# Kernel optimization log

Hardware: AMD Instinct MI355X
Metric: run time of the kernel (lower is better)

## Reference

```python
import jax, jax.numpy as jnp
import numpy as np

B, S, HID = 2, 2048, 1024
H = 16
D = HID // H  # 64
SCALE = 1.0 / float(np.sqrt(D))


def setup_inputs() -> dict:
    key = jax.random.key(0)
    ks = jax.random.split(key, 12)
    s = 0.02
    return {
        "query": jax.random.normal(ks[0], (B, S, HID), jnp.float32),
        "key": jax.random.normal(ks[1], (B, S, HID), jnp.float32),
        "value": jax.random.normal(ks[2], (B, S, HID), jnp.float32),
        "attention_mask": jnp.ones((B, S, S), jnp.int32),
        "Wq": jax.random.normal(ks[3], (HID, HID), jnp.float32) * s,
        "bq": jnp.zeros((HID,), jnp.float32),
        "Wk": jax.random.normal(ks[4], (HID, HID), jnp.float32) * s,
        "bk": jnp.zeros((HID,), jnp.float32),
        "Wv": jax.random.normal(ks[5], (HID, HID), jnp.float32) * s,
        "bv": jnp.zeros((HID,), jnp.float32),
        "Wo": jax.random.normal(ks[6], (HID, HID), jnp.float32) * s,
        "bo": jnp.zeros((HID,), jnp.float32),
    }


def _split_heads(x):  # [B,S,HID] -> [B,H,S,D]
    b, s, _ = x.shape
    return x.reshape(b, s, H, D).transpose(0, 2, 1, 3)


def reference(query, key, value, attention_mask, Wq, bq, Wk, bk, Wv, bv, Wo, bo):
    # Projections (torch Linear: x @ W.T + b)
    Q = _split_heads(query @ Wq.T + bq)
    K = _split_heads(key @ Wk.T + bk)
    V = _split_heads(value @ Wv.T + bv)
    # Full attention; chunking in the original is math-equivalent (softmax over full key axis per chunk)
    scores = jnp.einsum("bhqd,bhkd->bhqk", Q, K) * SCALE
    scores = jnp.where(attention_mask[:, None, :, :] == 0, jnp.float32(-1e9), scores)
    attn = jax.nn.softmax(scores, axis=-1)  # dropout is identity in eval mode
    ctx = jnp.einsum("bhqk,bhkd->bhqd", attn, V)
    ctx = ctx.transpose(0, 2, 1, 3).reshape(query.shape[0], query.shape[1], HID)
    out = ctx @ Wo.T + bo
    # module returns a dummy uniform attention-weight tensor
    attn_weights = jnp.full((query.shape[0], H, S, S), 1.0 / S, dtype=query.dtype)
    return (out, attn_weights)
```

## Files before the change

kernel.cpp:

```cpp
#include <hip/hip_runtime.h>

typedef float f4v __attribute__((ext_vector_type(4)));
typedef float f8v __attribute__((ext_vector_type(8)));
typedef short s4v __attribute__((ext_vector_type(4)));
typedef short s8v __attribute__((ext_vector_type(8)));
typedef __bf16 bf4t __attribute__((ext_vector_type(4)));
typedef __bf16 bf8t __attribute__((ext_vector_type(8)));
typedef unsigned short u16;
typedef unsigned int u32;

#define S_LEN 2048
#define HIDN 1024
#define NH 16
#define HD 64
#define QS 0.180336879f
#define DTH 11.5415603f
#define FILLV 0.00048828125f

__device__ __forceinline__ u16 f2bf(float f) {
  return __builtin_bit_cast(u16, (__bf16)f);
}

__device__ __forceinline__ s8v cvt8(f4v x, f4v y) {
  const f8v f = {x[0], x[1], x[2], x[3], y[0], y[1], y[2], y[3]};
  return __builtin_bit_cast(s8v, __builtin_convertvector(f, bf8t));
}

__device__ __forceinline__ s4v cvt4(f4v x) {
  return __builtin_bit_cast(s4v, __builtin_convertvector(x, bf4t));
}

__device__ __forceinline__ f4v mfma16(s8v a, s8v b, f4v c) {
  return __builtin_amdgcn_mfma_f32_16x16x32_bf16(
      __builtin_bit_cast(bf8t, a), __builtin_bit_cast(bf8t, b), c, 0, 0, 0);
}

__device__ __forceinline__ void gl16(const void* g, void* l) {
  __builtin_amdgcn_global_load_lds((const __attribute__((address_space(1))) u32*)g,
                                   (__attribute__((address_space(3))) u32*)l, 16, 0, 0);
}

#define FILL_DECL(nblk)                                        \
  const f4v fvv = (f4v){FILLV, FILLV, FILLV, FILLV};           \
  f4v* fp = fillb + (size_t)bid * 256 + threadIdx.x;           \
  f4v* const fpe = fillb + fill4;                               \
  const size_t FT = (size_t)(nblk) * 256;

#define FILL_STORE()                                           \
  do { if (fp < fpe) __builtin_nontemporal_store(fvv, fp);     \
       fp += FT; } while (0)

struct PrepArgs { const float* w[4]; u16* d[4]; const int* mask; unsigned* pm; unsigned* flg; };

__global__ __launch_bounds__(256) void prep(PrepArgs a) {
  const int y = blockIdx.y;
  const int tid = threadIdx.x;
  if (y < 4) {
    const float* s = a.w[y];
    u16* d = a.d[y];
#pragma unroll
    for (int j = 0; j < 2; ++j) {
      const int i = blockIdx.x * 256 + tid + j * 65536;
      const f4v x0 = ((const f4v*)s)[2 * i];
      const f4v x1 = ((const f4v*)s)[2 * i + 1];
      ((s8v*)d)[i] = cvt8(x0, x1);
    }
  } else {
    const int lane = tid & 63;
    const size_t base = (size_t)(y - 4) * 2097152;
    bool anyz = false;
    for (int j = 0; j < 32; ++j) {
      const size_t i = base + (size_t)blockIdx.x * 256 + tid + (size_t)j * 65536;
      const unsigned long long bb = __ballot(a.mask[i] != 0);
      if (lane == 0) a.pm[i >> 5] = (unsigned)bb;
      if (lane == 32) a.pm[i >> 5] = (unsigned)(bb >> 32);
      anyz |= (bb != ~0ull);
    }
    if (anyz && lane == 0) a.flg[0] = 1u;
  }
}

struct QkvArgs {
  const float* A[3]; const u16* W[3]; const float* bias[3]; u16* out[3];
  f4v* fillb; size_t fill4;
};

__global__ __launch_bounds__(256, 3) void gemm_qkv(QkvArgs ga) {
  __shared__ __align__(16) u16 As[128 * 32];
  __shared__ __align__(16) u16 Bs[128 * 32];
  const int p = blockIdx.x;
  const int xcd = p & 7;
  const int ii = p >> 3;
  const int ytile = xcd * 12 + (ii >> 3);
  const int xt = ii & 7;
  const int id = ytile >> 5;
  const int tid = threadIdx.x;
  const int lane = tid & 63;
  const int wv = tid >> 6;
  const int wm = wv >> 1, wn = wv & 1;
  const int g = lane >> 4, l15 = lane & 15;
  const int m0 = (ytile & 31) * 128, n0 = xt * 128;
  const int bid = p;
  f4v* fillb = ga.fillb;
  const size_t fill4 = ga.fill4;
  FILL_DECL(768);

  f4v acc[4][4];
#pragma unroll
  for (int i = 0; i < 4; ++i)
#pragma unroll
    for (int j = 0; j < 4; ++j) acc[i][j] = (f4v){0.f, 0.f, 0.f, 0.f};

  const int ar = tid >> 1;
  const int ac = (tid & 1) * 16;
  const float* ap = ga.A[id] + (size_t)(m0 + ar) * HIDN + ac;
  const u16* bp0 = ga.W[id] + (size_t)(n0 + (tid >> 2)) * HIDN + (tid & 3) * 8;
  const u16* bp1 = bp0 + (size_t)64 * HIDN;
  u16* bsl0 = Bs + tid * 8;
  u16* bsl1 = Bs + 2048 + tid * 8;
  u16* asl = As + ar * 32 + ac;

  for (int kt = 0; kt < HIDN; kt += 32) {
    const f4v a0 = ((const f4v*)(ap + kt))[0];
    const f4v a1 = ((const f4v*)(ap + kt))[1];
    const f4v a2 = ((const f4v*)(ap + kt))[2];
    const f4v a3 = ((const f4v*)(ap + kt))[3];
    __syncthreads();
    gl16(bp0 + kt, bsl0);
    gl16(bp1 + kt, bsl1);
    *(s8v*)asl = cvt8(a0, a1);
    *(s8v*)(asl + 8) = cvt8(a2, a3);
    __syncthreads();
    FILL_STORE();
    FILL_STORE();
    s8v af[4], bfv[4];
#pragma unroll
    for (int i = 0; i < 4; ++i)
      af[i] = *(const s8v*)(As + (wm * 64 + i * 16 + l15) * 32 + g * 8);
#pragma unroll
    for (int j = 0; j < 4; ++j)
      bfv[j] = *(const s8v*)(Bs + (wn * 64 + j * 16 + l15) * 32 + g * 8);
#pragma unroll
    for (int i = 0; i < 4; ++i)
#pragma unroll
      for (int j = 0; j < 4; ++j) acc[i][j] = mfma16(af[i], bfv[j], acc[i][j]);
  }

  const float* bias = ga.bias[id];
  u16* out = ga.out[id];
  const int mode2 = (id == 2);
  const float osc = (id == 0) ? QS : 1.0f;
#pragma unroll
  for (int i = 0; i < 4; ++i) {
#pragma unroll
    for (int j = 0; j < 4; ++j) {
      const int mb = m0 + wm * 64 + i * 16 + g * 4;
      const int n = n0 + wn * 64 + j * 16 + l15;
      const float bv = bias[n];
#pragma unroll
      for (int r = 0; r < 4; ++r) {
        const int m = mb + r;
        const float v = (acc[i][j][r] + bv) * osc;
        const int b = m >> 11, s = m & 2047, h = n >> 6, d = n & 63;
        if (mode2) {
          out[((size_t)(b * NH + h) * HD + d) * S_LEN + s] = f2bf(v);
        } else {
          out[(((size_t)(b * NH + h) * S_LEN + s) << 6) + d] = f2bf(v);
        }
      }
    }
  }
}

__global__ __launch_bounds__(256, 4) void attn_fused(
    const u16* __restrict__ Qb, const u16* __restrict__ Kb,
    const u16* __restrict__ Vtb, u16* __restrict__ ctxb,
    const unsigned* __restrict__ pm, const unsigned* __restrict__ flg,
    f4v* __restrict__ fillb, const size_t fill4) {
  __shared__ __align__(16) u16 Ks[64 * 64];
  __shared__ __align__(16) u16 Vs[64 * 64];
  __shared__ __align__(16) u16 Ps[4][16 * 64];
  __shared__ unsigned mw[64][2];

  const int p = blockIdx.x;
  const int xcd = p & 7;
  const int ii = p >> 3;
  const int bh = xcd * 4 + (ii >> 5);
  const int q0 = (ii & 31) * 64;
  const int tid = threadIdx.x;
  const int lane = tid & 63;
  const int wv = tid >> 6;
  const int g = lane >> 4, l15 = lane & 15;
  const int b = bh >> 4, h = bh & 15;
  const bool allones = (flg[0] == 0u);
  const int bid = p;
  FILL_DECL(1024);

  const u16* qp = Qb + ((size_t)bh * S_LEN + q0 + wv * 16 + l15) * HD + g * 8;
  const s8v qb0 = *(const s8v*)qp;
  const s8v qb1 = *(const s8v*)(qp + 32);

  f4v o[4];
#pragma unroll
  for (int nb = 0; nb < 4; ++nb) o[nb] = (f4v){0.f, 0.f, 0.f, 0.f};
  float mr = -INFINITY, lr = 0.f;

  const int sr = tid >> 3;
  const int sg = tid & 7;
  const int sc0 = ((sg ^ (sr & 7)) * 8);
  const u16* kp0 = Kb + ((size_t)bh * S_LEN + sr) * HD + sc0;
  const u16* kp1 = kp0 + (size_t)32 * HD;
  const u16* vp0 = Vtb + ((size_t)bh * HD + sr) * S_LEN + sc0;
  const u16* vp1 = vp0 + (size_t)32 * S_LEN;
  u16* kl = Ks + tid * 8;
  u16* vl = Vs + tid * 8;
  u16* pw = Ps[wv];

  for (int kt = 0; kt < S_LEN; kt += 64) {
    __syncthreads();
    gl16(kp0 + (size_t)kt * HD, kl);
    gl16(kp1 + (size_t)kt * HD, kl + 2048);
    gl16(vp0 + kt, vl);
    gl16(vp1 + kt, vl + 2048);
    if (!allones && tid < 128) {
      mw[tid >> 1][tid & 1] =
          pm[((size_t)b * S_LEN + q0 + (tid >> 1)) * (S_LEN / 32) + (kt >> 5) + (tid & 1)];
    }
    __syncthreads();
    FILL_STORE();
    FILL_STORE();

    f4v sc[4];
    __builtin_amdgcn_s_setprio(1);
#pragma unroll
    for (int nb = 0; nb < 4; ++nb) {
      const int kr = nb * 16 + l15;
      const s8v ka0 = *(const s8v*)(Ks + kr * 64 + ((g ^ (kr & 7)) * 8));
      const s8v ka1 = *(const s8v*)(Ks + kr * 64 + (((4 + g) ^ (kr & 7)) * 8));
      f4v z = (f4v){0.f, 0.f, 0.f, 0.f};
      z = mfma16(ka0, qb0, z);
      z = mfma16(ka1, qb1, z);
      sc[nb] = z;
    }
    __builtin_amdgcn_s_setprio(0);
    if (!allones) {
      const int qr = wv * 16 + l15;
      const unsigned w0 = mw[qr][0], w1 = mw[qr][1];
#pragma unroll
      for (int nb = 0; nb < 4; ++nb) {
        const unsigned wmk = (nb < 2) ? w0 : w1;
#pragma unroll
        for (int r = 0; r < 4; ++r) {
          const int bit = ((nb & 1) << 4) + (g << 2) + r;
          if (!((wmk >> bit) & 1u)) sc[nb][r] = -1e9f;
        }
      }
    }

    float tm = sc[0][0];
#pragma unroll
    for (int nb = 0; nb < 4; ++nb)
#pragma unroll
      for (int r = 0; r < 4; ++r) tm = fmaxf(tm, sc[nb][r]);
    tm = fmaxf(tm, __shfl_xor(tm, 16, 64));
    tm = fmaxf(tm, __shfl_xor(tm, 32, 64));
    if (!__all(tm <= mr + DTH)) {
      const float mn = fmaxf(mr, tm);
      const float al = exp2f(mr - mn);
      mr = mn;
      lr *= al;
#pragma unroll
      for (int r = 0; r < 4; ++r) {
        const float ar = __shfl(al, (g << 2) + r, 64);
#pragma unroll
        for (int nb = 0; nb < 4; ++nb) o[nb][r] *= ar;
      }
    }
    float rs = 0.f;
#pragma unroll
    for (int nb = 0; nb < 4; ++nb)
#pragma unroll
      for (int r = 0; r < 4; ++r) {
        const float p_ = exp2f(sc[nb][r] - mr);
        sc[nb][r] = p_;
        rs += p_;
      }
    rs += __shfl_xor(rs, 16, 64);
    rs += __shfl_xor(rs, 32, 64);
    lr += rs;
#pragma unroll
    for (int nb = 0; nb < 4; ++nb) {
      *(s4v*)(pw + l15 * 64 + ((nb * 16 + g * 4) ^ ((l15 & 7) * 8))) = cvt4(sc[nb]);
    }

    const s8v pa0 = *(const s8v*)(pw + l15 * 64 + ((g ^ (l15 & 7)) * 8));
    const s8v pa1 = *(const s8v*)(pw + l15 * 64 + (((4 + g) ^ (l15 & 7)) * 8));

    __builtin_amdgcn_s_setprio(1);
#pragma unroll
    for (int nb = 0; nb < 4; ++nb) {
      const int vr = nb * 16 + l15;
      const s8v vb0 = *(const s8v*)(Vs + vr * 64 + ((g ^ (vr & 7)) * 8));
      const s8v vb1 = *(const s8v*)(Vs + vr * 64 + (((4 + g) ^ (vr & 7)) * 8));
      o[nb] = mfma16(pa0, vb0, o[nb]);
      o[nb] = mfma16(pa1, vb1, o[nb]);
    }
    __builtin_amdgcn_s_setprio(0);
  }

#pragma unroll
  for (int r = 0; r < 4; ++r) {
    const float linv = 1.f / __shfl(lr, (g << 2) + r, 64);
    const int q = q0 + wv * 16 + g * 4 + r;
#pragma unroll
    for (int nb = 0; nb < 4; ++nb) {
      const int d = nb * 16 + l15;
      ctxb[(((size_t)b * S_LEN + q) * NH + h) * HD + d] = f2bf(o[nb][r] * linv);
    }
  }
}

__global__ __launch_bounds__(256, 4) void gemm_out(
    const u16* __restrict__ A, const u16* __restrict__ W,
    const float* __restrict__ bias, float* __restrict__ out,
    f4v* __restrict__ fillb, const size_t fill4) {
  __shared__ __align__(16) u16 As[128 * 32];
  __shared__ __align__(16) u16 Bs[64 * 32];
  const int p = blockIdx.x;
  const int xcd = p & 7;
  const int ii = p >> 3;
  const int m0 = (xcd * 4 + (ii >> 4)) * 128;
  const int n0 = (ii & 15) * 64;
  const int tid = threadIdx.x;
  const int lane = tid & 63;
  const int wv = tid >> 6;
  const int wm = wv >> 1, wn = wv & 1;
  const int g = lane >> 4, l15 = lane & 15;
  const int bid = p;
  FILL_DECL(512);

  f4v acc[4][2];
#pragma unroll
  for (int i = 0; i < 4; ++i)
#pragma unroll
    for (int j = 0; j < 2; ++j) acc[i][j] = (f4v){0.f, 0.f, 0.f, 0.f};

  const u16* ap0 = A + (size_t)(m0 + (tid >> 2)) * HIDN + (tid & 3) * 8;
  const u16* ap1 = ap0 + (size_t)64 * HIDN;
  const u16* bp0 = W + (size_t)(n0 + (tid >> 2)) * HIDN + (tid & 3) * 8;
  u16* asl0 = As + tid * 8;
  u16* asl1 = As + 2048 + tid * 8;
  u16* bsl0 = Bs + tid * 8;

  for (int kt = 0; kt < HIDN; kt += 32) {
    __syncthreads();
    gl16(ap0 + kt, asl0);
    gl16(ap1 + kt, asl1);
    gl16(bp0 + kt, bsl0);
    __syncthreads();
    FILL_STORE();
    s8v af[4], bfv[2];
#pragma unroll
    for (int i = 0; i < 4; ++i)
      af[i] = *(const s8v*)(As + (wm * 64 + i * 16 + l15) * 32 + g * 8);
#pragma unroll
    for (int j = 0; j < 2; ++j)
      bfv[j] = *(const s8v*)(Bs + (wn * 32 + j * 16 + l15) * 32 + g * 8);
#pragma unroll
    for (int i = 0; i < 4; ++i)
#pragma unroll
      for (int j = 0; j < 2; ++j) acc[i][j] = mfma16(af[i], bfv[j], acc[i][j]);
  }

#pragma unroll
  for (int i = 0; i < 4; ++i) {
#pragma unroll
    for (int j = 0; j < 2; ++j) {
      const int mb = m0 + wm * 64 + i * 16 + g * 4;
      const int n = n0 + wn * 32 + j * 16 + l15;
      const float bv = bias[n];
#pragma unroll
      for (int r = 0; r < 4; ++r) {
        out[(size_t)(mb + r) * HIDN + n] = acc[i][j][r] + bv;
      }
    }
  }
}

__global__ void fill_tail(float* __restrict__ p, const size_t n4) {
  const f4v v = (f4v){FILLV, FILLV, FILLV, FILLV};
  size_t i = (size_t)blockIdx.x * blockDim.x + threadIdx.x;
  const size_t st = (size_t)gridDim.x * blockDim.x;
  f4v* p4 = (f4v*)p;
  for (; i < n4; i += st) p4[i] = v;
}

extern "C" void kernel_launch(void* const* d_in, const int* in_sizes, int n_in,
                              void* d_out, int out_size, void* d_ws, size_t ws_size,
                              hipStream_t stream) {
  const float* query = (const float*)d_in[0];
  const float* key_ = (const float*)d_in[1];
  const float* value = (const float*)d_in[2];
  const int* amask = (const int*)d_in[3];
  const float* Wq = (const float*)d_in[4];
  const float* bq = (const float*)d_in[5];
  const float* Wk = (const float*)d_in[6];
  const float* bk = (const float*)d_in[7];
  const float* Wv = (const float*)d_in[8];
  const float* bv = (const float*)d_in[9];
  const float* Wo = (const float*)d_in[10];
  const float* bo = (const float*)d_in[11];

  float* out = (float*)d_out;
  const size_t OUT0 = (size_t)2 * S_LEN * HIDN;
  float* outw = out + OUT0;

  const size_t MB = (size_t)1 << 20;
  const size_t CARVE = 48 * MB;
  const bool use_ws = ws_size >= CARVE;
  char* scratch = use_ws ? (char*)d_ws : (char*)outw;

  u16* wq16 = (u16*)(scratch);
  u16* wk16 = (u16*)(scratch + 2 * MB);
  u16* wv16 = (u16*)(scratch + 4 * MB);
  u16* wo16 = (u16*)(scratch + 6 * MB);
  u16* Qb = (u16*)(scratch + 8 * MB);
  u16* Kb = (u16*)(scratch + 16 * MB);
  u16* Vtb = (u16*)(scratch + 24 * MB);
  u16* ctxb = (u16*)(scratch + 32 * MB);
  unsigned* pm = (unsigned*)(scratch + 40 * MB);
  unsigned* flg = (unsigned*)(scratch + 41 * MB);

  f4v* fillp;
  size_t F;
  if (use_ws) {
    fillp = (f4v*)outw;
    F = 33554432;
  } else {
    fillp = (f4v*)(outw + CARVE / 4);
    F = 33554432 - CARVE / 16;
  }
  const size_t capq = (size_t)768 * 256 * 64;
  const size_t capa = (size_t)1024 * 256 * 64;
  const size_t cq = F < capq ? F : capq;
  const size_t F1 = F - cq;
  const size_t ca = F1 < capa ? F1 : capa;
  const size_t co = F1 - ca;
  f4v* fq = fillp;
  f4v* fa = fq + cq;
  f4v* fo = fa + ca;

  hipMemsetAsync(flg, 0, 4, stream);

  PrepArgs pa;
  pa.w[0] = Wq; pa.w[1] = Wk; pa.w[2] = Wv; pa.w[3] = Wo;
  pa.d[0] = wq16; pa.d[1] = wk16; pa.d[2] = wv16; pa.d[3] = wo16;
  pa.mask = amask; pa.pm = pm; pa.flg = flg;
  prep<<<dim3(256, 8), 256, 0, stream>>>(pa);

  QkvArgs qa;
  qa.A[0] = query; qa.A[1] = key_; qa.A[2] = value;
  qa.W[0] = wq16; qa.W[1] = wk16; qa.W[2] = wv16;
  qa.bias[0] = bq; qa.bias[1] = bk; qa.bias[2] = bv;
  qa.out[0] = Qb; qa.out[1] = Kb; qa.out[2] = Vtb;
  qa.fillb = fq; qa.fill4 = cq;
  gemm_qkv<<<768, 256, 0, stream>>>(qa);

  attn_fused<<<1024, 256, 0, stream>>>(Qb, Kb, Vtb, ctxb, pm, flg, fa, ca);

  gemm_out<<<512, 256, 0, stream>>>(ctxb, wo16, bo, out, fo, co);

  if (!use_ws) {
    fill_tail<<<2048, 256, 0, stream>>>(outw, CARVE / 16);
  }
}
```

Measured before the change: 190.3 us.

## Double-buffer LDS tiles in QKV and output projection GEMMs

After: 197.6 us. 1.04x slower.

```diff
diff --git a/kernel.cpp b/kernel.cpp
--- a/kernel.cpp
+++ b/kernel.cpp
@@ -86,8 +86,8 @@
 };
 
 __global__ __launch_bounds__(256, 3) void gemm_qkv(QkvArgs ga) {
-  __shared__ __align__(16) u16 As[128 * 32];
-  __shared__ __align__(16) u16 Bs[128 * 32];
+  __shared__ __align__(16) u16 As[2 * 128 * 32];
+  __shared__ __align__(16) u16 Bs[2 * 128 * 32];
   const int p = blockIdx.x;
   const int xcd = p & 7;
   const int ii = p >> 3;
@@ -116,34 +116,51 @@
   const float* ap = ga.A[id] + (size_t)(m0 + ar) * HIDN + ac;
   const u16* bp0 = ga.W[id] + (size_t)(n0 + (tid >> 2)) * HIDN + (tid & 3) * 8;
   const u16* bp1 = bp0 + (size_t)64 * HIDN;
-  u16* bsl0 = Bs + tid * 8;
-  u16* bsl1 = Bs + 2048 + tid * 8;
-  u16* asl = As + ar * 32 + ac;
-
+
+  {
+    const f4v a0 = ((const f4v*)ap)[0];
+    const f4v a1 = ((const f4v*)ap)[1];
+    const f4v a2 = ((const f4v*)ap)[2];
+    const f4v a3 = ((const f4v*)ap)[3];
+    gl16(bp0, Bs + tid * 8);
+    gl16(bp1, Bs + 2048 + tid * 8);
+    *(s8v*)(As + ar * 32 + ac) = cvt8(a0, a1);
+    *(s8v*)(As + ar * 32 + ac + 8) = cvt8(a2, a3);
+  }
+
+  int cur = 0;
   for (int kt = 0; kt < HIDN; kt += 32) {
-    const f4v a0 = ((const f4v*)(ap + kt))[0];
-    const f4v a1 = ((const f4v*)(ap + kt))[1];
-    const f4v a2 = ((const f4v*)(ap + kt))[2];
-    const f4v a3 = ((const f4v*)(ap + kt))[3];
+    const int ktn = kt + 32;
+    const bool more = ktn < HIDN;
+    const float* apn = ap + (more ? ktn : kt);
+    const f4v a0 = ((const f4v*)apn)[0];
+    const f4v a1 = ((const f4v*)apn)[1];
+    const f4v a2 = ((const f4v*)apn)[2];
+    const f4v a3 = ((const f4v*)apn)[3];
     __syncthreads();
-    gl16(bp0 + kt, bsl0);
-    gl16(bp1 + kt, bsl1);
-    *(s8v*)asl = cvt8(a0, a1);
-    *(s8v*)(asl + 8) = cvt8(a2, a3);
-    __syncthreads();
+    const int nxt = cur ^ 1;
+    if (more) {
+      gl16(bp0 + ktn, Bs + nxt * 4096 + tid * 8);
+      gl16(bp1 + ktn, Bs + nxt * 4096 + 2048 + tid * 8);
+      *(s8v*)(As + nxt * 4096 + ar * 32 + ac) = cvt8(a0, a1);
+      *(s8v*)(As + nxt * 4096 + ar * 32 + ac + 8) = cvt8(a2, a3);
+    }
     FILL_STORE();
     FILL_STORE();
+    const u16* Ab = As + cur * 4096;
+    const u16* Bb = Bs + cur * 4096;
     s8v af[4], bfv[4];
 #pragma unroll
     for (int i = 0; i < 4; ++i)
-      af[i] = *(const s8v*)(As + (wm * 64 + i * 16 + l15) * 32 + g * 8);
+      af[i] = *(const s8v*)(Ab + (wm * 64 + i * 16 + l15) * 32 + g * 8);
 #pragma unroll
     for (int j = 0; j < 4; ++j)
-      bfv[j] = *(const s8v*)(Bs + (wn * 64 + j * 16 + l15) * 32 + g * 8);
+      bfv[j] = *(const s8v*)(Bb + (wn * 64 + j * 16 + l15) * 32 + g * 8);
 #pragma unroll
     for (int i = 0; i < 4; ++i)
 #pragma unroll
       for (int j = 0; j < 4; ++j) acc[i][j] = mfma16(af[i], bfv[j], acc[i][j]);
+    cur = nxt;
   }
 
   const float* bias = ga.bias[id];
@@ -324,8 +341,8 @@
     const u16* __restrict__ A, const u16* __restrict__ W,
     const float* __restrict__ bias, float* __restrict__ out,
     f4v* __restrict__ fillb, const size_t fill4) {
-  __shared__ __align__(16) u16 As[128 * 32];
-  __shared__ __align__(16) u16 Bs[64 * 32];
+  __shared__ __align__(16) u16 As[2 * 128 * 32];
+  __shared__ __align__(16) u16 Bs[2 * 64 * 32];
   const int p = blockIdx.x;
   const int xcd = p & 7;
   const int ii = p >> 3;
@@ -348,28 +365,37 @@
   const u16* ap0 = A + (size_t)(m0 + (tid >> 2)) * HIDN + (tid & 3) * 8;
   const u16* ap1 = ap0 + (size_t)64 * HIDN;
   const u16* bp0 = W + (size_t)(n0 + (tid >> 2)) * HIDN + (tid & 3) * 8;
-  u16* asl0 = As + tid * 8;
-  u16* asl1 = As + 2048 + tid * 8;
-  u16* bsl0 = Bs + tid * 8;
-
+
+  gl16(ap0, As + tid * 8);
+  gl16(ap1, As + 2048 + tid * 8);
+  gl16(bp0, Bs + tid * 8);
+
+  int cur = 0;
   for (int kt = 0; kt < HIDN; kt += 32) {
+    const int ktn = kt + 32;
+    const bool more = ktn < HIDN;
     __syncthreads();
-    gl16(ap0 + kt, asl0);
-    gl16(ap1 + kt, asl1);
-    gl16(bp0 + kt, bsl0);
-    __syncthreads();
+    const int nxt = cur ^ 1;
+    if (more) {
+      gl16(ap0 + ktn, As + nxt * 4096 + tid * 8);
+      gl16(ap1 + ktn, As + nxt * 4096 + 2048 + tid * 8);
+      gl16(bp0 + ktn, Bs + nxt * 2048 + tid * 8);
+    }
     FILL_STORE();
+    const u16* Ab = As + cur * 4096;
+    const u16* Bb = Bs + cur * 2048;
     s8v af[4], bfv[2];
 #pragma unroll
     for (int i = 0; i < 4; ++i)
-      af[i] = *(const s8v*)(As + (wm * 64 + i * 16 + l15) * 32 + g * 8);
+      af[i] = *(const s8v*)(Ab + (wm * 64 + i * 16 + l15) * 32 + g * 8);
 #pragma unroll
     for (int j = 0; j < 2; ++j)
-      bfv[j] = *(const s8v*)(Bs + (wn * 32 + j * 16 + l15) * 32 + g * 8);
+      bfv[j] = *(const s8v*)(Bb + (wn * 32 + j * 16 + l15) * 32 + g * 8);
 #pragma unroll
     for (int i = 0; i < 4; ++i)
 #pragma unroll
       for (int j = 0; j < 2; ++j) acc[i][j] = mfma16(af[i], bfv[j], acc[i][j]);
+    cur = nxt;
   }
 
 #pragma unroll
```

## Drop prep kernel: convert weights in-GEMM and fold mask packing into QKV launch

Applied to the files above, without the earlier changes.

Result: slower. 265.5 us (+39.5%).

```diff
diff --git a/kernel.cpp b/kernel.cpp
--- a/kernel.cpp
+++ b/kernel.cpp
@@ -50,51 +50,37 @@
   do { if (fp < fpe) __builtin_nontemporal_store(fvv, fp);     \
        fp += FT; } while (0)
 
-struct PrepArgs { const float* w[4]; u16* d[4]; const int* mask; unsigned* pm; unsigned* flg; };
-
-__global__ __launch_bounds__(256) void prep(PrepArgs a) {
-  const int y = blockIdx.y;
-  const int tid = threadIdx.x;
-  if (y < 4) {
-    const float* s = a.w[y];
-    u16* d = a.d[y];
-#pragma unroll
-    for (int j = 0; j < 2; ++j) {
-      const int i = blockIdx.x * 256 + tid + j * 65536;
-      const f4v x0 = ((const f4v*)s)[2 * i];
-      const f4v x1 = ((const f4v*)s)[2 * i + 1];
-      ((s8v*)d)[i] = cvt8(x0, x1);
-    }
-  } else {
-    const int lane = tid & 63;
-    const size_t base = (size_t)(y - 4) * 2097152;
-    bool anyz = false;
-    for (int j = 0; j < 32; ++j) {
-      const size_t i = base + (size_t)blockIdx.x * 256 + tid + (size_t)j * 65536;
-      const unsigned long long bb = __ballot(a.mask[i] != 0);
-      if (lane == 0) a.pm[i >> 5] = (unsigned)bb;
-      if (lane == 32) a.pm[i >> 5] = (unsigned)(bb >> 32);
-      anyz |= (bb != ~0ull);
-    }
-    if (anyz && lane == 0) a.flg[0] = 1u;
-  }
-}
-
 struct QkvArgs {
-  const float* A[3]; const u16* W[3]; const float* bias[3]; u16* out[3];
+  const float* A[3]; const float* W[3]; const float* bias[3]; u16* out[3];
+  const int* mask; unsigned* pm; unsigned* flg;
   f4v* fillb; size_t fill4;
 };
 
 __global__ __launch_bounds__(256, 3) void gemm_qkv(QkvArgs ga) {
+  const int p = blockIdx.x;
+  const int tid = threadIdx.x;
+  if (p >= 768) {
+    const int mb = p - 768;
+    const int lane = tid & 63;
+    bool anyz = false;
+#pragma unroll
+    for (int j = 0; j < 256; ++j) {
+      const size_t i = (size_t)mb * 65536 + (size_t)j * 256 + tid;
+      const unsigned long long bb = __ballot(ga.mask[i] != 0);
+      if (lane == 0) ga.pm[i >> 5] = (unsigned)bb;
+      if (lane == 32) ga.pm[i >> 5] = (unsigned)(bb >> 32);
+      anyz |= (bb != ~0ull);
+    }
+    if (anyz && lane == 0) ga.flg[0] = 1u;
+    return;
+  }
   __shared__ __align__(16) u16 As[128 * 32];
   __shared__ __align__(16) u16 Bs[128 * 32];
-  const int p = blockIdx.x;
   const int xcd = p & 7;
   const int ii = p >> 3;
   const int ytile = xcd * 12 + (ii >> 3);
   const int xt = ii & 7;
   const int id = ytile >> 5;
-  const int tid = threadIdx.x;
   const int lane = tid & 63;
   const int wv = tid >> 6;
   const int wm = wv >> 1, wn = wv & 1;
@@ -114,22 +100,24 @@
   const int ar = tid >> 1;
   const int ac = (tid & 1) * 16;
   const float* ap = ga.A[id] + (size_t)(m0 + ar) * HIDN + ac;
-  const u16* bp0 = ga.W[id] + (size_t)(n0 + (tid >> 2)) * HIDN + (tid & 3) * 8;
-  const u16* bp1 = bp0 + (size_t)64 * HIDN;
-  u16* bsl0 = Bs + tid * 8;
-  u16* bsl1 = Bs + 2048 + tid * 8;
+  const float* bp = ga.W[id] + (size_t)(n0 + ar) * HIDN + ac;
   u16* asl = As + ar * 32 + ac;
+  u16* bsl = Bs + ar * 32 + ac;
 
   for (int kt = 0; kt < HIDN; kt += 32) {
     const f4v a0 = ((const f4v*)(ap + kt))[0];
     const f4v a1 = ((const f4v*)(ap + kt))[1];
     const f4v a2 = ((const f4v*)(ap + kt))[2];
     const f4v a3 = ((const f4v*)(ap + kt))[3];
-    __syncthreads();
-    gl16(bp0 + kt, bsl0);
-    gl16(bp1 + kt, bsl1);
+    const f4v b0 = ((const f4v*)(bp + kt))[0];
+    const f4v b1 = ((const f4v*)(bp + kt))[1];
+    const f4v b2 = ((const f4v*)(bp + kt))[2];
+    const f4v b3 = ((const f4v*)(bp + kt))[3];
+    __syncthreads();
     *(s8v*)asl = cvt8(a0, a1);
     *(s8v*)(asl + 8) = cvt8(a2, a3);
+    *(s8v*)bsl = cvt8(b0, b1);
+    *(s8v*)(bsl + 8) = cvt8(b2, b3);
     __syncthreads();
     FILL_STORE();
     FILL_STORE();
@@ -321,7 +309,7 @@
 }
 
 __global__ __launch_bounds__(256, 4) void gemm_out(
-    const u16* __restrict__ A, const u16* __restrict__ W,
+    const u16* __restrict__ A, const float* __restrict__ W,
     const float* __restrict__ bias, float* __restrict__ out,
     f4v* __restrict__ fillb, const size_t fill4) {
   __shared__ __align__(16) u16 As[128 * 32];
@@ -347,16 +335,18 @@
 
   const u16* ap0 = A + (size_t)(m0 + (tid >> 2)) * HIDN + (tid & 3) * 8;
   const u16* ap1 = ap0 + (size_t)64 * HIDN;
-  const u16* bp0 = W + (size_t)(n0 + (tid >> 2)) * HIDN + (tid & 3) * 8;
+  const float* bp = W + (size_t)(n0 + (tid >> 2)) * HIDN + (tid & 3) * 8;
   u16* asl0 = As + tid * 8;
   u16* asl1 = As + 2048 + tid * 8;
-  u16* bsl0 = Bs + tid * 8;
+  u16* bsl = Bs + (tid >> 2) * 32 + (tid & 3) * 8;
 
   for (int kt = 0; kt < HIDN; kt += 32) {
+    const f4v b0 = ((const f4v*)(bp + kt))[0];
+    const f4v b1 = ((const f4v*)(bp + kt))[1];
     __syncthreads();
     gl16(ap0 + kt, asl0);
     gl16(ap1 + kt, asl1);
-    gl16(bp0 + kt, bsl0);
+    *(s8v*)bsl = cvt8(b0, b1);
     __syncthreads();
     FILL_STORE();
     s8v af[4], bfv[2];
@@ -420,10 +410,6 @@
   const bool use_ws = ws_size >= CARVE;
   char* scratch = use_ws ? (char*)d_ws : (char*)outw;
 
-  u16* wq16 = (u16*)(scratch);
-  u16* wk16 = (u16*)(scratch + 2 * MB);
-  u16* wv16 = (u16*)(scratch + 4 * MB);
-  u16* wo16 = (u16*)(scratch + 6 * MB);
   u16* Qb = (u16*)(scratch + 8 * MB);
   u16* Kb = (u16*)(scratch + 16 * MB);
   u16* Vtb = (u16*)(scratch + 24 * MB);
@@ -452,23 +438,18 @@
 
   hipMemsetAsync(flg, 0, 4, stream);
 
-  PrepArgs pa;
-  pa.w[0] = Wq; pa.w[1] = Wk; pa.w[2] = Wv; pa.w[3] = Wo;
-  pa.d[0] = wq16; pa.d[1] = wk16; pa.d[2] = wv16; pa.d[3] = wo16;
-  pa.mask = amask; pa.pm = pm; pa.flg = flg;
-  prep<<<dim3(256, 8), 256, 0, stream>>>(pa);
-
   QkvArgs qa;
   qa.A[0] = query; qa.A[1] = key_; qa.A[2] = value;
-  qa.W[0] = wq16; qa.W[1] = wk16; qa.W[2] = wv16;
+  qa.W[0] = Wq; qa.W[1] = Wk; qa.W[2] = Wv;
   qa.bias[0] = bq; qa.bias[1] = bk; qa.bias[2] = bv;
   qa.out[0] = Qb; qa.out[1] = Kb; qa.out[2] = Vtb;
+  qa.mask = amask; qa.pm = pm; qa.flg = flg;
   qa.fillb = fq; qa.fill4 = cq;
-  gemm_qkv<<<768, 256, 0, stream>>>(qa);
+  gemm_qkv<<<896, 256, 0, stream>>>(qa);
 
   attn_fused<<<1024, 256, 0, stream>>>(Qb, Kb, Vtb, ctxb, pm, flg, fa, ca);
 
-  gemm_out<<<512, 256, 0, stream>>>(ctxb, wo16, bo, out, fo, co);
+  gemm_out<<<512, 256, 0, stream>>>(ctxb, Wo, bo, out, fo, co);
 
   if (!use_ws) {
     fill_tail<<<2048, 256, 0, stream>>>(outw, CARVE / 16);
```
